# Kernel tuning notes

Hardware: AMD Instinct MI355X
Metric: run time of the kernel (lower is better)

Reference implementation:

```python
import jax, jax.numpy as jnp
import numpy as np

N = 50000
E = 1600000
IN_DIM = 128
H = 8
D = 16  # out_dim per head


def setup_inputs() -> dict:
    key = jax.random.key(0)
    ks = jax.random.split(key, 9)
    h = jax.random.normal(ks[0], (N, IN_DIM), dtype=jnp.float32)
    src = jax.random.randint(ks[1], (E,), 0, N, dtype=jnp.int32)
    dst = jax.random.randint(ks[2], (E,), 0, N, dtype=jnp.int32)
    s = 1.0 / np.sqrt(IN_DIM)
    WQ = jax.random.uniform(ks[3], (IN_DIM, H * D), jnp.float32, -s, s)
    WK = jax.random.uniform(ks[4], (IN_DIM, H * D), jnp.float32, -s, s)
    WV = jax.random.uniform(ks[5], (IN_DIM, H * D), jnp.float32, -s, s)
    bQ = jax.random.uniform(ks[6], (H * D,), jnp.float32, -s, s)
    bK = jax.random.uniform(ks[7], (H * D,), jnp.float32, -s, s)
    bV = jax.random.uniform(ks[8], (H * D,), jnp.float32, -s, s)
    return {"h": h, "src": src, "dst": dst, "WQ": WQ, "WK": WK, "WV": WV,
            "bQ": bQ, "bK": bK, "bV": bV}


def reference(h, src, dst, WQ, WK, WV, bQ, bK, bV):
    # Node projections -> [N, H, D]
    Q = (h @ WQ + bQ).reshape(-1, H, D)
    K = (h @ WK + bK).reshape(-1, H, D)
    V = (h @ WV + bV).reshape(-1, H, D)
    # Edge scores: dot(K[src], Q[dst]) per head, scaled+clamped exp -> [E, H]
    scale = jnp.float32(np.sqrt(D))
    score = jnp.exp(jnp.clip(jnp.sum(K[src] * Q[dst], axis=-1) / scale, -5.0, 5.0))
    # Scatter-sum to destination nodes
    wV = jax.ops.segment_sum(score[:, :, None] * V[src], dst, num_segments=N)  # [N, H, D]
    z = jax.ops.segment_sum(score, dst, num_segments=N)  # [N, H]
    return wV / z[:, :, None]
```

## Files before the change

kernel.cpp:

```cpp
#include <hip/hip_runtime.h>

#define N_NODES 50000
#define N_PAD   50048
#define N_EDGES 1600000
#define HD 128
#define CHUNK 4096
#define NCHUNK ((N_EDGES + CHUNK - 1) / CHUNK)
#define NBUCKET ((N_NODES + 127) / 128)

typedef __attribute__((ext_vector_type(8))) short short8;
typedef __attribute__((ext_vector_type(4))) float floatx4;

union U4S8 { uint4 u; short8 s; };

__device__ __forceinline__ unsigned short f2bf(float f) {
    unsigned u = __float_as_uint(f);
    unsigned r = (u + 0x7fffu + ((u >> 16) & 1u)) >> 16;
    return (unsigned short)r;
}

__global__ __launch_bounds__(256) void k_chunkhist(
    const int* __restrict__ dst, int* __restrict__ chunkhist, int* __restrict__ btot,
    const float* __restrict__ WQ, const float* __restrict__ WK, const float* __restrict__ WV,
    unsigned short* __restrict__ Wf) {
    int t = threadIdx.x, c = blockIdx.x;
    if (c >= NCHUNK) {
        int tid = (c - NCHUNK) * 256 + t;
        int lane = tid & 63;
        int kstep = (tid >> 6) & 3;
        int ntile = tid >> 8;
        int g = ntile >> 3;
        int col = (ntile & 7) * 16 + (lane & 15);
        int k0 = kstep * 32 + (lane >> 4) * 8;
        const float* W = (g == 0) ? WQ : (g == 1) ? WK : WV;
        unsigned short r[8];
#pragma unroll
        for (int j = 0; j < 8; ++j)
            r[j] = f2bf(W[(size_t)(k0 + j) * HD + col]);
        *(uint4*)(Wf + (size_t)tid * 8) = *(uint4*)r;
        return;
    }
    __shared__ int hist[NBUCKET];
    for (int i = t; i < NBUCKET; i += 256) hist[i] = 0;
    __syncthreads();
    int e0 = c * CHUNK;
    int cnt = min(CHUNK, N_EDGES - e0);
    const uint4* d4 = (const uint4*)(dst + e0);
    int cnt4 = cnt >> 2;
    for (int i = t; i < cnt4; i += 256) {
        uint4 v = d4[i];
        atomicAdd(&hist[v.x >> 7], 1);
        atomicAdd(&hist[v.y >> 7], 1);
        atomicAdd(&hist[v.z >> 7], 1);
        atomicAdd(&hist[v.w >> 7], 1);
    }
    __syncthreads();
    for (int i = t; i < NBUCKET; i += 256) {
        int v = hist[i];
        chunkhist[c * NBUCKET + i] = v;
        if (v) atomicAdd(&btot[i], v);
    }
}

__global__ __launch_bounds__(256) void k_choff(const int* __restrict__ chunkhist,
                                               const int* __restrict__ btot,
                                               int* __restrict__ bucket_ptr,
                                               int* __restrict__ chunkoff) {
    int b = blockIdx.x, t = threadIdx.x;
    int x = 0;
    for (int i = t; i < NBUCKET; i += 256)
        if (i < b) x += btot[i];
    __shared__ int red[256];
    red[t] = x;
    __syncthreads();
    for (int off = 128; off > 0; off >>= 1) {
        if (t < off) red[t] += red[t + off];
        __syncthreads();
    }
    int base = red[0];
    if (t == 0) {
        bucket_ptr[b] = base;
        if (b == NBUCKET - 1) bucket_ptr[NBUCKET] = base + btot[b];
    }
    const int PER = (NCHUNK + 255) / 256;
    int c0 = t * PER;
    int v[PER];
    int s = 0;
#pragma unroll
    for (int i = 0; i < PER; ++i) {
        int c = c0 + i;
        v[i] = (c < NCHUNK) ? chunkhist[c * NBUCKET + b] : 0;
        s += v[i];
    }
    __shared__ int part[256];
    part[t] = s;
    __syncthreads();
    for (int off = 1; off < 256; off <<= 1) {
        int y = (t >= off) ? part[t - off] : 0;
        __syncthreads();
        part[t] += y;
        __syncthreads();
    }
    int run = base + part[t] - s;
#pragma unroll
    for (int i = 0; i < PER; ++i) {
        int c = c0 + i;
        if (c < NCHUNK) { chunkoff[c * NBUCKET + b] = run; run += v[i]; }
    }
}

__global__ __launch_bounds__(256) void k_scatter(const int* __restrict__ src,
                                                 const int* __restrict__ dst,
                                                 const int* __restrict__ chunkoff,
                                                 int* __restrict__ packed) {
    __shared__ int cur[NBUCKET];
    int t = threadIdx.x, c = blockIdx.x;
    for (int i = t; i < NBUCKET; i += 256) cur[i] = chunkoff[c * NBUCKET + i];
    __syncthreads();
    int e0 = c * CHUNK;
    int cnt = min(CHUNK, N_EDGES - e0);
    const uint4* d4 = (const uint4*)(dst + e0);
    const uint4* s4 = (const uint4*)(src + e0);
    int cnt4 = cnt >> 2;
    for (int i = t; i < cnt4; i += 256) {
        uint4 d = d4[i];
        uint4 s = s4[i];
        int pos;
        pos = atomicAdd(&cur[d.x >> 7], 1); packed[pos] = (s.x << 7) | (d.x & 127);
        pos = atomicAdd(&cur[d.y >> 7], 1); packed[pos] = (s.y << 7) | (d.y & 127);
        pos = atomicAdd(&cur[d.z >> 7], 1); packed[pos] = (s.z << 7) | (d.z & 127);
        pos = atomicAdd(&cur[d.w >> 7], 1); packed[pos] = (s.w << 7) | (d.w & 127);
    }
}

__global__ __launch_bounds__(256) void k_finalize(const int* __restrict__ bucket_ptr,
                                                  const int* __restrict__ packed,
                                                  int* __restrict__ row_ptr,
                                                  int* __restrict__ col_src) {
    __shared__ int hist[128], part[128], cur[128];
    int b = blockIdx.x, t = threadIdx.x;
    if (t < 128) hist[t] = 0;
    __syncthreads();
    int ebeg = bucket_ptr[b], eend = bucket_ptr[b + 1];
    int m = eend - ebeg;
    for (int i = t; i < m; i += 256)
        atomicAdd(&hist[packed[ebeg + i] & 127], 1);
    __syncthreads();
    int v = 0;
    if (t < 128) { v = hist[t]; part[t] = v; }
    __syncthreads();
    for (int off = 1; off < 128; off <<= 1) {
        int x = 0;
        if (t < 128 && t >= off) x = part[t - off];
        __syncthreads();
        if (t < 128) part[t] += x;
        __syncthreads();
    }
    if (t < 128) {
        int excl = part[t] - v;
        int node = b * 128 + t;
        if (node < N_NODES) row_ptr[node] = ebeg + excl;
        if (node == N_NODES - 1) row_ptr[N_NODES] = eend;
        cur[t] = ebeg + excl;
    }
    __syncthreads();
    for (int i = t; i < m; i += 256) {
        int p = packed[ebeg + i];
        int pos = atomicAdd(&cur[p & 127], 1);
        col_src[pos] = p >> 7;
    }
}


__global__ __launch_bounds__(256) void proj_mfma(
    const float* __restrict__ h, const unsigned short* __restrict__ Wf,
    const float* __restrict__ bQ, const float* __restrict__ bK, const float* __restrict__ bV,
    float* __restrict__ Qh, unsigned short* __restrict__ KV) {
    int t = threadIdx.x;
    int w = t >> 6;
    int l = t & 63;
    int row0 = blockIdx.x * 64 + w * 16;
    int arow = row0 + (l & 15);
    int akoff = (l >> 4) * 8;
    bool rowok = arow < N_NODES;

    short8 a[4];
#pragma unroll
    for (int ks = 0; ks < 4; ++ks) {
        unsigned short r[8];
        if (rowok) {
            const float4* ap = (const float4*)(h + (size_t)arow * HD + ks * 32 + akoff);
            float4 f0 = ap[0], f1 = ap[1];
            r[0] = f2bf(f0.x); r[1] = f2bf(f0.y); r[2] = f2bf(f0.z); r[3] = f2bf(f0.w);
            r[4] = f2bf(f1.x); r[5] = f2bf(f1.y); r[6] = f2bf(f1.z); r[7] = f2bf(f1.w);
        } else {
#pragma unroll
            for (int j = 0; j < 8; ++j) r[j] = 0;
        }
        a[ks] = *(short8*)r;
    }

    int orow0 = row0 + (l >> 4) * 4;
#pragma unroll
    for (int nt = 0; nt < 24; ++nt) {
        floatx4 acc = (floatx4){0.f, 0.f, 0.f, 0.f};
#pragma unroll
        for (int ks = 0; ks < 4; ++ks) {
            U4S8 u;
            u.u = *(const uint4*)(Wf + ((size_t)(nt * 4 + ks) * 64 + l) * 8);
            acc = __builtin_amdgcn_mfma_f32_16x16x32_bf16(a[ks], u.s, acc, 0, 0, 0);
        }
        int g = nt >> 3;
        int head = nt & 7;
        int ci = l & 15;
        float bias = (g == 0) ? bQ[head * 16 + ci] : (g == 1) ? bK[head * 16 + ci] : bV[head * 16 + ci];
#pragma unroll
        for (int r = 0; r < 4; ++r) {
            int grow = orow0 + r;
            if (grow < N_NODES) {
                float val = acc[r] + bias;
                size_t node_off = (size_t)head * N_PAD + grow;
                if (g == 0)      Qh[node_off * 16 + ci] = val;
                else if (g == 1) KV[node_off * 32 + ci] = f2bf(val);
                else             KV[node_off * 32 + 16 + ci] = f2bf(val);
            }
        }
    }
}


__device__ __forceinline__ float blo(unsigned u) { return __uint_as_float(u << 16); }
__device__ __forceinline__ float bhi(unsigned u) { return __uint_as_float(u & 0xffff0000u); }

__global__ __launch_bounds__(256) void attn_kernel(
    const float* __restrict__ Qh, const unsigned short* __restrict__ KV,
    const int* __restrict__ row_ptr, const int* __restrict__ col_src,
    float* __restrict__ out) {
    int head = blockIdx.x & 7;
    int grp  = blockIdx.x >> 3;
    int w = threadIdx.x >> 6;
    int l = threadIdx.x & 63;
    int q = l >> 3;
    int s = l & 7;
    int n = grp * 32 + w * 8 + q;
    bool nok = n < N_NODES;

    const float4* qp = (const float4*)(Qh + ((size_t)head * N_PAD + n) * 16);
    float4 q0 = qp[0], q1 = qp[1], q2 = qp[2], q3 = qp[3];

    float acc[16];
#pragma unroll
    for (int j = 0; j < 16; ++j) acc[j] = 0.f;
    float z = 0.f;

    int beg = 0, end = 0;
    if (nok) { beg = row_ptr[n]; end = row_ptr[n + 1]; }
    const unsigned short* KVh = KV + (size_t)head * N_PAD * 32;

    int e = beg + s;
    int idx0 = col_src[(e < end) ? e : beg];
    const uint4* rp = (const uint4*)(KVh + (size_t)idx0 * 32);
    uint4 c0 = rp[0], c1 = rp[1], c2 = rp[2], c3 = rp[3];

    while (e < end) {
        int e2 = e + 8;
        int idxn = col_src[(e2 < end) ? e2 : beg];
        const uint4* np = (const uint4*)(KVh + (size_t)idxn * 32);
        uint4 n0 = np[0], n1 = np[1], n2 = np[2], n3 = np[3];

        float dot = blo(c0.x) * q0.x + bhi(c0.x) * q0.y
                  + blo(c0.y) * q0.z + bhi(c0.y) * q0.w
                  + blo(c0.z) * q1.x + bhi(c0.z) * q1.y
                  + blo(c0.w) * q1.z + bhi(c0.w) * q1.w
                  + blo(c1.x) * q2.x + bhi(c1.x) * q2.y
                  + blo(c1.y) * q2.z + bhi(c1.y) * q2.w
                  + blo(c1.z) * q3.x + bhi(c1.z) * q3.y
                  + blo(c1.w) * q3.z + bhi(c1.w) * q3.w;
        float sc = __expf(fminf(fmaxf(dot * 0.25f, -5.f), 5.f));
        acc[0]  = fmaf(sc, blo(c2.x), acc[0]);
        acc[1]  = fmaf(sc, bhi(c2.x), acc[1]);
        acc[2]  = fmaf(sc, blo(c2.y), acc[2]);
        acc[3]  = fmaf(sc, bhi(c2.y), acc[3]);
        acc[4]  = fmaf(sc, blo(c2.z), acc[4]);
        acc[5]  = fmaf(sc, bhi(c2.z), acc[5]);
        acc[6]  = fmaf(sc, blo(c2.w), acc[6]);
        acc[7]  = fmaf(sc, bhi(c2.w), acc[7]);
        acc[8]  = fmaf(sc, blo(c3.x), acc[8]);
        acc[9]  = fmaf(sc, bhi(c3.x), acc[9]);
        acc[10] = fmaf(sc, blo(c3.y), acc[10]);
        acc[11] = fmaf(sc, bhi(c3.y), acc[11]);
        acc[12] = fmaf(sc, blo(c3.z), acc[12]);
        acc[13] = fmaf(sc, bhi(c3.z), acc[13]);
        acc[14] = fmaf(sc, blo(c3.w), acc[14]);
        acc[15] = fmaf(sc, bhi(c3.w), acc[15]);
        z += sc;
        c0 = n0; c1 = n1; c2 = n2; c3 = n3;
        e = e2;
    }

#pragma unroll
    for (int j = 0; j < 16; ++j) {
        acc[j] += __shfl_xor(acc[j], 1);
        acc[j] += __shfl_xor(acc[j], 2);
        acc[j] += __shfl_xor(acc[j], 4);
    }
    z += __shfl_xor(z, 1);
    z += __shfl_xor(z, 2);
    z += __shfl_xor(z, 4);

    if (s == 0 && nok) {
        float inv = 1.f / z;
        float* O = out + (size_t)n * HD + head * 16;
        ((float4*)O)[0] = (float4){acc[0] * inv,  acc[1] * inv,  acc[2] * inv,  acc[3] * inv};
        ((float4*)O)[1] = (float4){acc[4] * inv,  acc[5] * inv,  acc[6] * inv,  acc[7] * inv};
        ((float4*)O)[2] = (float4){acc[8] * inv,  acc[9] * inv,  acc[10] * inv, acc[11] * inv};
        ((float4*)O)[3] = (float4){acc[12] * inv, acc[13] * inv, acc[14] * inv, acc[15] * inv};
    }
}


static inline char* align256(char* p) {
    return (char*)(((uintptr_t)p + 255) & ~(uintptr_t)255);
}

extern "C" void kernel_launch(void* const* d_in, const int* in_sizes, int n_in,
                              void* d_out, int out_size, void* d_ws, size_t ws_size,
                              hipStream_t stream) {
    const float* h  = (const float*)d_in[0];
    const int*   src = (const int*)d_in[1];
    const int*   dst = (const int*)d_in[2];
    const float* WQ = (const float*)d_in[3];
    const float* WK = (const float*)d_in[4];
    const float* WV = (const float*)d_in[5];
    const float* bQ = (const float*)d_in[6];
    const float* bK = (const float*)d_in[7];
    const float* bV = (const float*)d_in[8];
    float* out = (float*)d_out;

    char* p = (char*)d_ws;
    float* Qh = (float*)p;                   p += (size_t)8 * N_PAD * 16 * 4;
    unsigned short* KV = (unsigned short*)p; p += (size_t)8 * N_PAD * 32 * 2;
    unsigned short* Wf = (unsigned short*)p; p += (size_t)24 * 4 * 64 * 8 * 2;
    p = align256(p);
    int* row_ptr    = (int*)p;               p += (N_NODES + 2) * 4;
    p = align256(p);
    int* bucket_ptr = (int*)p;               p += (NBUCKET + 1) * 4;
    p = align256(p);
    int* btot       = (int*)p;               p += NBUCKET * 4;
    p = align256(p);
    int* chunkhist  = (int*)p;               p += (size_t)NCHUNK * NBUCKET * 4;
    p = align256(p);
    int* chunkoff   = (int*)p;               p += (size_t)NCHUNK * NBUCKET * 4;
    p = align256(p);
    int* packed     = (int*)p;               p += (size_t)N_EDGES * 4;
    p = align256(p);
    int* col_src    = (int*)p;               p += (size_t)N_EDGES * 4;

    (void)hipMemsetAsync(btot, 0, NBUCKET * sizeof(int), stream);
    k_chunkhist<<<NCHUNK + 24, 256, 0, stream>>>(dst, chunkhist, btot, WQ, WK, WV, Wf);
    k_choff<<<NBUCKET, 256, 0, stream>>>(chunkhist, btot, bucket_ptr, chunkoff);
    k_scatter<<<NCHUNK, 256, 0, stream>>>(src, dst, chunkoff, packed);
    k_finalize<<<NBUCKET, 256, 0, stream>>>(bucket_ptr, packed, row_ptr, col_src);
    proj_mfma<<<N_PAD / 64, 256, 0, stream>>>(h, Wf, bQ, bK, bV, Qh, KV);
    int grps = (N_NODES + 31) / 32;
    attn_kernel<<<grps * 8, 256, 0, stream>>>(Qh, KV, row_ptr, col_src, out);
}
```

Baseline: 272.2 us.

## Fuse projection into histogram launch, halve chunk size, deepen index prefetch

The memset and the weight conversion move into a small prep kernel. The MFMA projection blocks now run inside the same launch as the destination-histogram chunks, so the two independent stages overlap and one launch is removed. The chunk size drops from 4096 to 2048 edges, which gives more histogram and scatter blocks but a larger per-chunk histogram table. The attention loop now prefetches the column index two iterations ahead to hide the dependent index-then-row load latency, at the cost of one more register and extra kernel complexity.

```diff
diff --git a/kernel.cpp b/kernel.cpp
--- a/kernel.cpp
+++ b/kernel.cpp
@@ -4,9 +4,10 @@
 #define N_PAD   50048
 #define N_EDGES 1600000
 #define HD 128
-#define CHUNK 4096
+#define CHUNK 2048
 #define NCHUNK ((N_EDGES + CHUNK - 1) / CHUNK)
 #define NBUCKET ((N_NODES + 127) / 128)
+#define PROJ_BLOCKS (N_PAD / 64)
 
 typedef __attribute__((ext_vector_type(8))) short short8;
 typedef __attribute__((ext_vector_type(4))) float floatx4;
@@ -19,13 +20,12 @@
     return (unsigned short)r;
 }
 
-__global__ __launch_bounds__(256) void k_chunkhist(
-    const int* __restrict__ dst, int* __restrict__ chunkhist, int* __restrict__ btot,
+__global__ __launch_bounds__(256) void k_prep(
     const float* __restrict__ WQ, const float* __restrict__ WK, const float* __restrict__ WV,
-    unsigned short* __restrict__ Wf) {
-    int t = threadIdx.x, c = blockIdx.x;
-    if (c >= NCHUNK) {
-        int tid = (c - NCHUNK) * 256 + t;
+    unsigned short* __restrict__ Wf, int* __restrict__ btot) {
+    int bid = blockIdx.x, t = threadIdx.x;
+    if (bid < 24) {
+        int tid = bid * 256 + t;
         int lane = tid & 63;
         int kstep = (tid >> 6) & 3;
         int ntile = tid >> 8;
@@ -38,6 +38,75 @@
         for (int j = 0; j < 8; ++j)
             r[j] = f2bf(W[(size_t)(k0 + j) * HD + col]);
         *(uint4*)(Wf + (size_t)tid * 8) = *(uint4*)r;
+    } else {
+        for (int i = t; i < NBUCKET; i += 256) btot[i] = 0;
+    }
+}
+
+__device__ __forceinline__ void proj_body(
+    int bid, int t,
+    const float* __restrict__ h, const unsigned short* __restrict__ Wf,
+    const float* __restrict__ bQ, const float* __restrict__ bK, const float* __restrict__ bV,
+    float* __restrict__ Qh, unsigned short* __restrict__ KV) {
+    int w = t >> 6;
+    int l = t & 63;
+    int row0 = bid * 64 + w * 16;
+    int arow = row0 + (l & 15);
+    int akoff = (l >> 4) * 8;
+    bool rowok = arow < N_NODES;
+
+    short8 a[4];
+#pragma unroll
+    for (int ks = 0; ks < 4; ++ks) {
+        unsigned short r[8];
+        if (rowok) {
+            const float4* ap = (const float4*)(h + (size_t)arow * HD + ks * 32 + akoff);
+            float4 f0 = ap[0], f1 = ap[1];
+            r[0] = f2bf(f0.x); r[1] = f2bf(f0.y); r[2] = f2bf(f0.z); r[3] = f2bf(f0.w);
+            r[4] = f2bf(f1.x); r[5] = f2bf(f1.y); r[6] = f2bf(f1.z); r[7] = f2bf(f1.w);
+        } else {
+#pragma unroll
+            for (int j = 0; j < 8; ++j) r[j] = 0;
+        }
+        a[ks] = *(short8*)r;
+    }
+
+    int orow0 = row0 + (l >> 4) * 4;
+#pragma unroll
+    for (int nt = 0; nt < 24; ++nt) {
+        floatx4 acc = (floatx4){0.f, 0.f, 0.f, 0.f};
+#pragma unroll
+        for (int ks = 0; ks < 4; ++ks) {
+            U4S8 u;
+            u.u = *(const uint4*)(Wf + ((size_t)(nt * 4 + ks) * 64 + l) * 8);
+            acc = __builtin_amdgcn_mfma_f32_16x16x32_bf16(a[ks], u.s, acc, 0, 0, 0);
+        }
+        int g = nt >> 3;
+        int head = nt & 7;
+        int ci = l & 15;
+        float bias = (g == 0) ? bQ[head * 16 + ci] : (g == 1) ? bK[head * 16 + ci] : bV[head * 16 + ci];
+#pragma unroll
+        for (int r = 0; r < 4; ++r) {
+            int grow = orow0 + r;
+            if (grow < N_NODES) {
+                float val = acc[r] + bias;
+                size_t node_off = (size_t)head * N_PAD + grow;
+                if (g == 0)      Qh[node_off * 16 + ci] = val;
+                else if (g == 1) KV[node_off * 32 + ci] = f2bf(val);
+                else             KV[node_off * 32 + 16 + ci] = f2bf(val);
+            }
+        }
+    }
+}
+
+__global__ __launch_bounds__(256) void k_hist_proj(
+    const int* __restrict__ dst, int* __restrict__ chunkhist, int* __restrict__ btot,
+    const float* __restrict__ h, const unsigned short* __restrict__ Wf,
+    const float* __restrict__ bQ, const float* __restrict__ bK, const float* __restrict__ bV,
+    float* __restrict__ Qh, unsigned short* __restrict__ KV) {
+    int t = threadIdx.x, c = blockIdx.x;
+    if (c >= NCHUNK) {
+        proj_body(c - NCHUNK, t, h, Wf, bQ, bK, bV, Qh, KV);
         return;
     }
     __shared__ int hist[NBUCKET];
@@ -172,63 +241,6 @@
 }
 
 
-__global__ __launch_bounds__(256) void proj_mfma(
-    const float* __restrict__ h, const unsigned short* __restrict__ Wf,
-    const float* __restrict__ bQ, const float* __restrict__ bK, const float* __restrict__ bV,
-    float* __restrict__ Qh, unsigned short* __restrict__ KV) {
-    int t = threadIdx.x;
-    int w = t >> 6;
-    int l = t & 63;
-    int row0 = blockIdx.x * 64 + w * 16;
-    int arow = row0 + (l & 15);
-    int akoff = (l >> 4) * 8;
-    bool rowok = arow < N_NODES;
-
-    short8 a[4];
-#pragma unroll
-    for (int ks = 0; ks < 4; ++ks) {
-        unsigned short r[8];
-        if (rowok) {
-            const float4* ap = (const float4*)(h + (size_t)arow * HD + ks * 32 + akoff);
-            float4 f0 = ap[0], f1 = ap[1];
-            r[0] = f2bf(f0.x); r[1] = f2bf(f0.y); r[2] = f2bf(f0.z); r[3] = f2bf(f0.w);
-            r[4] = f2bf(f1.x); r[5] = f2bf(f1.y); r[6] = f2bf(f1.z); r[7] = f2bf(f1.w);
-        } else {
-#pragma unroll
-            for (int j = 0; j < 8; ++j) r[j] = 0;
-        }
-        a[ks] = *(short8*)r;
-    }
-
-    int orow0 = row0 + (l >> 4) * 4;
-#pragma unroll
-    for (int nt = 0; nt < 24; ++nt) {
-        floatx4 acc = (floatx4){0.f, 0.f, 0.f, 0.f};
-#pragma unroll
-        for (int ks = 0; ks < 4; ++ks) {
-            U4S8 u;
-            u.u = *(const uint4*)(Wf + ((size_t)(nt * 4 + ks) * 64 + l) * 8);
-            acc = __builtin_amdgcn_mfma_f32_16x16x32_bf16(a[ks], u.s, acc, 0, 0, 0);
-        }
-        int g = nt >> 3;
-        int head = nt & 7;
-        int ci = l & 15;
-        float bias = (g == 0) ? bQ[head * 16 + ci] : (g == 1) ? bK[head * 16 + ci] : bV[head * 16 + ci];
-#pragma unroll
-        for (int r = 0; r < 4; ++r) {
-            int grow = orow0 + r;
-            if (grow < N_NODES) {
-                float val = acc[r] + bias;
-                size_t node_off = (size_t)head * N_PAD + grow;
-                if (g == 0)      Qh[node_off * 16 + ci] = val;
-                else if (g == 1) KV[node_off * 32 + ci] = f2bf(val);
-                else             KV[node_off * 32 + 16 + ci] = f2bf(val);
-            }
-        }
-    }
-}
-
-
 __device__ __forceinline__ float blo(unsigned u) { return __uint_as_float(u << 16); }
 __device__ __forceinline__ float bhi(unsigned u) { return __uint_as_float(u & 0xffff0000u); }
 
@@ -257,17 +269,18 @@
     if (nok) { beg = row_ptr[n]; end = row_ptr[n + 1]; }
     const unsigned short* KVh = KV + (size_t)head * N_PAD * 32;
 
-    int e = beg + s;
-    int idx0 = col_src[(e < end) ? e : beg];
-    const uint4* rp = (const uint4*)(KVh + (size_t)idx0 * 32);
+    int e0 = beg + s;
+    int e1 = e0 + 8;
+    int i1 = col_src[e1 < end ? e1 : beg];
+    int ic = col_src[e0 < end ? e0 : beg];
+    const uint4* rp = (const uint4*)(KVh + (size_t)ic * 32);
     uint4 c0 = rp[0], c1 = rp[1], c2 = rp[2], c3 = rp[3];
 
-    while (e < end) {
-        int e2 = e + 8;
-        int idxn = col_src[(e2 < end) ? e2 : beg];
-        const uint4* np = (const uint4*)(KVh + (size_t)idxn * 32);
+    for (int e = e0; e < end; e += 8) {
+        const uint4* np = (const uint4*)(KVh + (size_t)i1 * 32);
         uint4 n0 = np[0], n1 = np[1], n2 = np[2], n3 = np[3];
-
+        int e2 = e + 16;
+        int i2 = col_src[e2 < end ? e2 : beg];
         float dot = blo(c0.x) * q0.x + bhi(c0.x) * q0.y
                   + blo(c0.y) * q0.z + bhi(c0.y) * q0.w
                   + blo(c0.z) * q1.x + bhi(c0.z) * q1.y
@@ -295,7 +308,7 @@
         acc[15] = fmaf(sc, bhi(c3.w), acc[15]);
         z += sc;
         c0 = n0; c1 = n1; c2 = n2; c3 = n3;
-        e = e2;
+        i1 = i2;
     }
 
 #pragma unroll
@@ -356,12 +369,12 @@
     p = align256(p);
     int* col_src    = (int*)p;               p += (size_t)N_EDGES * 4;
 
-    (void)hipMemsetAsync(btot, 0, NBUCKET * sizeof(int), stream);
-    k_chunkhist<<<NCHUNK + 24, 256, 0, stream>>>(dst, chunkhist, btot, WQ, WK, WV, Wf);
+    k_prep<<<25, 256, 0, stream>>>(WQ, WK, WV, Wf, btot);
+    k_hist_proj<<<NCHUNK + PROJ_BLOCKS, 256, 0, stream>>>(
+        dst, chunkhist, btot, h, Wf, bQ, bK, bV, Qh, KV);
     k_choff<<<NBUCKET, 256, 0, stream>>>(chunkhist, btot, bucket_ptr, chunkoff);
     k_scatter<<<NCHUNK, 256, 0, stream>>>(src, dst, chunkoff, packed);
     k_finalize<<<NBUCKET, 256, 0, stream>>>(bucket_ptr, packed, row_ptr, col_src);
-    proj_mfma<<<N_PAD / 64, 256, 0, stream>>>(h, Wf, bQ, bK, bV, Qh, KV);
     int grps = (N_NODES + 31) / 32;
     attn_kernel<<<grps * 8, 256, 0, stream>>>(Qh, KV, row_ptr, col_src, out);
 }
```

Result: slower. 279.6 us (+2.7%).
